# Kernel tuning notes

Measured on AMD Instinct MI355X. Metric: run time of the kernel, lower is better.

## Reference

```python
import jax, jax.numpy as jnp
import numpy as np

D_MODEL = 2048
D_STATE = 64
D_CONV = 4
EXPAND = 2
HEADDIM = 64
NGROUPS = 1
CHUNK = 64
D_INNER = EXPAND * D_MODEL            # 4096
NHEADS = D_INNER // HEADDIM           # 64
D_XBC = D_INNER + 2 * NGROUPS * D_STATE
D_IN_PROJ = 2 * D_INNER + 2 * NGROUPS * D_STATE + NHEADS


def setup_inputs():
    key = jax.random.key(0)
    ks = jax.random.split(key, 8)
    B, L = 2, 4096
    u = jax.random.normal(ks[0], (B, L, D_MODEL), jnp.float32)
    W_in = jax.random.normal(ks[1], (D_IN_PROJ, D_MODEL), jnp.float32) * 0.02
    conv_w = jax.random.normal(ks[2], (D_XBC, D_CONV), jnp.float32) * 0.2
    conv_b = jnp.zeros((D_XBC,), jnp.float32)
    dt = jnp.exp(jax.random.uniform(ks[3], (NHEADS,)) * (np.log(0.1) - np.log(0.001)) + np.log(0.001))
    dt = jnp.clip(dt, 1e-4)
    dt_bias = dt + jnp.log(-jnp.expm1(-dt))
    A_log = jnp.log(jax.random.uniform(ks[4], (NHEADS,), minval=1.0, maxval=16.0))
    D_param = jnp.ones((NHEADS,), jnp.float32)
    norm_w = jnp.ones((D_INNER,), jnp.float32)
    W_out = jax.random.normal(ks[5], (D_MODEL, D_INNER), jnp.float32) * 0.02
    return dict(u=u, W_in=W_in, conv_w=conv_w, conv_b=conv_b, dt_bias=dt_bias,
                A_log=A_log, D_param=D_param, norm_w=norm_w, W_out=W_out)


def segsum(x):
    # x: (..., T) -> (..., T, T) with entry [l,s] = sum_{s< i <= l} x[i], -inf above diag
    T = x.shape[-1]
    mask_strict = jnp.tril(jnp.ones((T, T), bool), k=-1)
    mask_incl = jnp.tril(jnp.ones((T, T), bool), k=0)
    xe = jnp.where(mask_strict, x[..., :, None], 0.0)  # element [l,s] = x[l] if l>s
    xseg = jnp.cumsum(xe, axis=-2)
    return jnp.where(mask_incl, xseg, -jnp.inf)


def ssd_scan(X, A, Bm, Cm, block_len=CHUNK):
    # X: (b,L,h,p), A: (b,L,h), Bm/Cm: (b,L,h,n)
    b, seqlen, h, p = X.shape
    n = Bm.shape[-1]
    pad_len = (block_len - seqlen % block_len) % block_len
    if pad_len > 0:
        X = jnp.pad(X, ((0, 0), (0, pad_len), (0, 0), (0, 0)))
        A = jnp.pad(A, ((0, 0), (0, pad_len), (0, 0)))
        Bm = jnp.pad(Bm, ((0, 0), (0, pad_len), (0, 0), (0, 0)))
        Cm = jnp.pad(Cm, ((0, 0), (0, pad_len), (0, 0), (0, 0)))
    L = X.shape[1]
    c = L // block_len
    Xc = X.reshape(b, c, block_len, h, p)
    Ac = A.reshape(b, c, block_len, h).transpose(0, 3, 1, 2)  # (b,h,c,l)
    Bc = Bm.reshape(b, c, block_len, h, n)
    Cc = Cm.reshape(b, c, block_len, h, n)
    A_cum = jnp.cumsum(Ac, axis=-1)                           # (b,h,c,l)
    Lmat = jnp.exp(segsum(Ac))                                # (b,h,c,l,s)
    CB = jnp.einsum('bclhn,bcshn->bhcls', Cc, Bc)
    Y_diag = jnp.einsum('bhcls,bcshp->bhclp', CB * Lmat, Xc)
    decay_states = jnp.exp(A_cum[..., -1:] - A_cum)           # (b,h,c,l)
    states = jnp.einsum('bhcl,bclhn,bclhp->bhcpn', decay_states, Bc, Xc)
    init = jnp.zeros((b, h, 1, p, n), X.dtype)
    states = jnp.concatenate([init, states], axis=2)          # (b,h,c+1,p,n)
    chunk_decay = jnp.pad(A_cum[..., -1], ((0, 0), (0, 0), (1, 0)))  # (b,h,c+1)
    decay_chunk = jnp.exp(segsum(chunk_decay))                # (b,h,c+1,c+1)
    new_states = jnp.einsum('bhzc,bhcpn->bhzpn', decay_chunk, states)[:, :, :-1]
    Y_off = jnp.einsum('bclhn,bhcpn,bhcl->bhclp', Cc, new_states, jnp.exp(A_cum))
    Y = (Y_diag + Y_off).transpose(0, 2, 3, 1, 4).reshape(b, L, h, p)
    if pad_len > 0:
        Y = Y[:, :seqlen]
    return Y


def rmsnorm_grouped(x, w, ngroups, eps=1e-5):
    gs = x.shape[-1] // ngroups
    xg = x.reshape(*x.shape[:-1], ngroups, gs)
    xg = xg * jax.lax.rsqrt(jnp.mean(xg * xg, axis=-1, keepdims=True) + eps)
    return xg.reshape(x.shape) * w


def reference(u, W_in, conv_w, conv_b, dt_bias, A_log, D_param, norm_w, W_out):
    B, L, _ = u.shape
    zxbcdt = u @ W_in.T                                      # (B,L,d_in_proj)
    z = zxbcdt[..., :D_INNER]
    xBC = zxbcdt[..., D_INNER:D_INNER + D_XBC]
    dt = zxbcdt[..., D_INNER + D_XBC:]
    # causal depthwise conv1d, kernel D_CONV, left-pad D_CONV-1
    xpad = jnp.pad(xBC, ((0, 0), (D_CONV - 1, 0), (0, 0)))
    conv = conv_b
    for k in range(D_CONV):
        conv = conv + conv_w[:, k] * xpad[:, k:k + L, :]
    xBC = jax.nn.silu(conv)
    x = xBC[..., :D_INNER].reshape(B, L, NHEADS, HEADDIM)
    B_ssm = xBC[..., D_INNER:D_INNER + NGROUPS * D_STATE].reshape(B, L, NGROUPS, D_STATE)
    C_ssm = xBC[..., D_INNER + NGROUPS * D_STATE:].reshape(B, L, NGROUPS, D_STATE)
    if NGROUPS < NHEADS:
        rep = NHEADS // NGROUPS
        B_ssm = jnp.repeat(B_ssm, rep, axis=2)
        C_ssm = jnp.repeat(C_ssm, rep, axis=2)
    dt = jax.nn.softplus(dt + dt_bias)                        # (B,L,nheads)
    A = -jnp.exp(A_log)                                       # (nheads,)
    y = ssd_scan(x * dt[..., None], A * dt, B_ssm, C_ssm, block_len=CHUNK)
    y = y + D_param[:, None] * x
    y = y.reshape(B, L, D_INNER)
    y = rmsnorm_grouped(y * jax.nn.silu(z), norm_w, NGROUPS)
    return y @ W_out.T
```

## Files before the change

### kernel.cpp

```cpp
#include <hip/hip_runtime.h>
#include <hip/hip_bf16.h>
#include <math.h>

#define SEQ       4096
#define DMODEL    2048
#define DINNER    4096
#define DXBC      4224
#define NPROJ     8384
#define NHEADS    64
#define HDIM      64
#define DSTATE    64
#define NCHUNK    64
#define XLD       4352

typedef __attribute__((ext_vector_type(8))) _Float16 half8;
typedef __attribute__((ext_vector_type(2))) _Float16 half2v;
typedef __attribute__((ext_vector_type(4))) float floatx4;

__device__ __forceinline__ void async_copy16(void* lds, const void* g) {
  __builtin_amdgcn_global_load_lds(
      (const __attribute__((address_space(1))) unsigned int*)g,
      (__attribute__((address_space(3))) unsigned int*)lds, 16, 0, 0);
}

__device__ __forceinline__ float silu_f(float x) { return x / (1.f + __expf(-x)); }

__device__ __forceinline__ void cvt8(const float* __restrict__ s, _Float16* __restrict__ d) {
  float4 a = *(const float4*)s;
  float4 b = *(const float4*)(s + 4);
  half8 h;
  h[0] = (_Float16)a.x; h[1] = (_Float16)a.y; h[2] = (_Float16)a.z; h[3] = (_Float16)a.w;
  h[4] = (_Float16)b.x; h[5] = (_Float16)b.y; h[6] = (_Float16)b.z; h[7] = (_Float16)b.w;
  *(half8*)d = h;
}

__global__ void diag_kernel(float* out, float v) { out[0] = v; }

__global__ void cvt8_kernel(const float* __restrict__ src, _Float16* __restrict__ dst, int n8) {
  int i = blockIdx.x * 256 + threadIdx.x;
  if (i < n8) cvt8(src + (size_t)i * 8, dst + (size_t)i * 8);
}

#define U_N8 (SEQ * DMODEL / 8)
__global__ void cvt_in_kernel(const float* __restrict__ u, const float* __restrict__ W_in,
                              _Float16* __restrict__ ubf, _Float16* __restrict__ winbf) {
  int i = blockIdx.x * 256 + threadIdx.x;
  if (i < U_N8) {
    cvt8(u + (size_t)i * 8, ubf + (size_t)i * 8);
  } else {
    int j = i - U_N8;
    int row = j >> 8;
    size_t off = (size_t)j * 8;
    if (row < NPROJ) {
      cvt8(W_in + off, winbf + off);
    } else {
      half8 zz = {};
      *(half8*)(winbf + off) = zz;
    }
  }
}

template <typename OT>
__global__ __launch_bounds__(256) void gemm_bt64(
    const _Float16* __restrict__ A, const _Float16* __restrict__ B,
    OT* __restrict__ C0, OT* __restrict__ C1, int K,
    int ldc0, int ldc1, int ncol0, int tiles_m, int tiles_n) {
  __shared__ __align__(16) _Float16 As[128 * 64];
  __shared__ __align__(16) _Float16 Bs[128 * 64];
  int t = threadIdx.x;
  int nt = tiles_m * tiles_n;
  int id = blockIdx.x;
  int id2 = ((nt & 7) == 0) ? ((id & 7) * (nt >> 3) + (id >> 3)) : id;
  int wband = tiles_m << 2;
  int g = id2 / wband;
  int rm = id2 - g * wband;
  int bw = tiles_n - (g << 2); if (bw > 4) bw = 4;
  int pn = (g << 2) + rm % bw;
  int pm = rm / bw;
  int m0 = pm * 128, n0 = pn * 128;

  int w = t >> 6, lane = t & 63, q = lane >> 4, r = lane & 15;
  int wm = (w >> 1) * 64, wn = (w & 1) * 64;
  int rowoff = lane >> 3;
  int chunkoff = ((lane & 7) ^ rowoff) * 8;
  const _Float16* gA[4];
  const _Float16* gB[4];
#pragma unroll
  for (int i = 0; i < 4; ++i) {
    gA[i] = A + (size_t)(m0 + i * 32 + w * 8 + rowoff) * K + chunkoff;
    gB[i] = B + (size_t)(n0 + i * 32 + w * 8 + rowoff) * K + chunkoff;
  }
  floatx4 acc[4][4] = {};
  for (int k0 = 0; k0 < K; k0 += 64) {
#pragma unroll
    for (int i = 0; i < 4; ++i) {
      async_copy16(As + (i * 32 + w * 8) * 64, gA[i] + k0);
      async_copy16(Bs + (i * 32 + w * 8) * 64, gB[i] + k0);
    }
    __syncthreads();
#pragma unroll
    for (int kk = 0; kk < 64; kk += 32) {
      half8 af[4], bf[4];
#pragma unroll
      for (int im = 0; im < 4; ++im) {
        int R = wm + im * 16 + r;
        af[im] = *(const half8*)&As[R * 64 + ((((kk >> 3) + q) ^ (R & 7)) << 3)];
      }
#pragma unroll
      for (int in = 0; in < 4; ++in) {
        int R = wn + in * 16 + r;
        bf[in] = *(const half8*)&Bs[R * 64 + ((((kk >> 3) + q) ^ (R & 7)) << 3)];
      }
#pragma unroll
      for (int im = 0; im < 4; ++im)
#pragma unroll
        for (int in = 0; in < 4; ++in)
          acc[im][in] =
              __builtin_amdgcn_mfma_f32_16x16x32_f16(af[im], bf[in], acc[im][in], 0, 0, 0);
    }
    __syncthreads();
  }
  OT* Cp = (n0 < ncol0) ? C0 : C1;
  int ldc = (n0 < ncol0) ? ldc0 : ldc1;
  int cb = (n0 < ncol0) ? n0 : n0 - ncol0;
#pragma unroll
  for (int im = 0; im < 4; ++im)
#pragma unroll
    for (int in = 0; in < 4; ++in)
#pragma unroll
      for (int i = 0; i < 4; ++i)
        Cp[(size_t)(m0 + wm + im * 16 + q * 4 + i) * ldc + cb + wn + in * 16 + r] =
            (OT)acc[im][in][i];
}

template <typename OT>
__global__ __launch_bounds__(512, 2) void gemm256(
    const _Float16* __restrict__ A, const _Float16* __restrict__ B,
    OT* __restrict__ C, int K, int ldc, int tiles_m, int tiles_n) {
  __shared__ __align__(16) _Float16 As[2][256 * 64];
  __shared__ __align__(16) _Float16 Bs[2][256 * 64];
  int t = threadIdx.x;
  int nwg = tiles_m * tiles_n;
  int id = blockIdx.x;
  int wgid = ((nwg & 7) == 0) ? ((id & 7) * (nwg >> 3) + (id >> 3)) : id;
  int wband = tiles_m << 2;
  int g = wgid / wband;
  int rm = wgid - g * wband;
  int bw = tiles_n - (g << 2); if (bw > 4) bw = 4;
  int pn = (g << 2) + rm % bw;
  int pm = rm / bw;
  int m0 = pm * 256, n0 = pn * 256;

  int w = t >> 6, lane = t & 63, q4 = lane >> 4, r16 = lane & 15;
  int wm = (w >> 2) * 128, wn = (w & 3) * 64;
  int srow = lane >> 3;
  int schunk = ((lane & 7) ^ srow) << 3;
  const _Float16* gA0 = A + (size_t)(m0 + w * 8 + srow) * K + schunk;
  const _Float16* gB0 = B + (size_t)(n0 + w * 8 + srow) * K + schunk;

  floatx4 acc[8][4] = {};

  auto STAGE = [&](int buf, int kt) {
    int k0 = kt << 6;
#pragma unroll
    for (int i = 0; i < 4; ++i) {
      async_copy16(&As[buf][(i * 64 + w * 8) * 64], gA0 + (size_t)(i * 64) * K + k0);
      async_copy16(&Bs[buf][(i * 64 + w * 8) * 64], gB0 + (size_t)(i * 64) * K + k0);
    }
  };

  int NT = K >> 6;
  STAGE(0, 0);
  STAGE(1, 1);
  asm volatile("s_waitcnt vmcnt(8)" ::: "memory");
  __builtin_amdgcn_s_barrier();
  asm volatile("" ::: "memory");

  for (int kt = 0; kt < NT; ++kt) {
    int cur = kt & 1;
    const _Float16* Ab = As[cur];
    const _Float16* Bb = Bs[cur];
#define RD(buf_, R_, kk_) \
  (*(const half8*)&buf_[(R_) * 64 + (((((kk_) >> 3) + q4) ^ ((R_) & 7)) << 3)])
#define PHASE(qm, qn)                                                          \
    {                                                                          \
      half8 af[4][2], bf[2][2];                                                \
      _Pragma("unroll") for (int m = 0; m < 4; ++m) {                          \
        int R = wm + ((qm) * 4 + m) * 16 + r16;                                \
        af[m][0] = RD(Ab, R, 0);                                               \
        af[m][1] = RD(Ab, R, 32);                                              \
      }                                                                        \
      _Pragma("unroll") for (int n = 0; n < 2; ++n) {                          \
        int R = wn + ((qn) * 2 + n) * 16 + r16;                                \
        bf[n][0] = RD(Bb, R, 0);                                               \
        bf[n][1] = RD(Bb, R, 32);                                              \
      }                                                                        \
      __builtin_amdgcn_s_setprio(1);                                           \
      _Pragma("unroll") for (int m = 0; m < 4; ++m)                            \
        _Pragma("unroll") for (int n = 0; n < 2; ++n) {                        \
          acc[(qm) * 4 + m][(qn) * 2 + n] = __builtin_amdgcn_mfma_f32_16x16x32_f16( \
              af[m][0], bf[n][0], acc[(qm) * 4 + m][(qn) * 2 + n], 0, 0, 0);   \
          acc[(qm) * 4 + m][(qn) * 2 + n] = __builtin_amdgcn_mfma_f32_16x16x32_f16( \
              af[m][1], bf[n][1], acc[(qm) * 4 + m][(qn) * 2 + n], 0, 0, 0);   \
        }                                                                      \
      __builtin_amdgcn_s_setprio(0);                                           \
    }
    PHASE(0, 0) PHASE(1, 0) PHASE(1, 1) PHASE(0, 1)
#undef PHASE
#undef RD
    if (kt + 1 < NT) {
      asm volatile("s_waitcnt lgkmcnt(0)" ::: "memory");
      __builtin_amdgcn_s_barrier();
      asm volatile("" ::: "memory");
      if (kt + 2 < NT) {
        STAGE(cur, kt + 2);
        asm volatile("s_waitcnt vmcnt(8)" ::: "memory");
      } else {
        asm volatile("s_waitcnt vmcnt(0)" ::: "memory");
      }
      __builtin_amdgcn_s_barrier();
      asm volatile("" ::: "memory");
    }
  }
#pragma unroll
  for (int m = 0; m < 8; ++m)
#pragma unroll
    for (int n = 0; n < 4; ++n)
#pragma unroll
      for (int i = 0; i < 4; ++i)
        C[(size_t)(m0 + wm + m * 16 + q4 * 4 + i) * ldc + n0 + wn + n * 16 + r16] =
            (OT)acc[m][n][i];
}

#define CONVB (SEQ * (DXBC / 2) / 256)
__global__ __launch_bounds__(256) void conv_dtscan_kernel(
    const _Float16* __restrict__ xin, const float* __restrict__ conv_w,
    const float* __restrict__ conv_b, _Float16* __restrict__ xcv,
    const float* __restrict__ dt_bias, const float* __restrict__ A_log,
    float* __restrict__ dtp, float* __restrict__ acum, float* __restrict__ chs) {
  int t = threadIdx.x;
  if (blockIdx.x < CONVB) {
    int idx = blockIdx.x * 256 + t;
    int l = idx / (DXBC / 2);
    int c = (idx - l * (DXBC / 2)) * 2;
    const _Float16* zc = xin + (size_t)l * XLD + c;
    float a0 = conv_b[c], a1 = conv_b[c + 1];
#pragma unroll
    for (int k = 0; k < 4; ++k) {
      int off = k - 3;
      if (l + off >= 0) {
        half2v v = *(const half2v*)(zc + (long)off * XLD);
        a0 += conv_w[c * 4 + k] * (float)v[0];
        a1 += conv_w[c * 4 + 4 + k] * (float)v[1];
      }
    }
    half2v o;
    o[0] = (_Float16)silu_f(a0);
    o[1] = (_Float16)silu_f(a1);
    *(half2v*)(xcv + (size_t)l * DXBC + c) = o;
  } else {
    __shared__ float dAs[64 * 65];
    int c = blockIdx.x - CONVB;
    int h = t & 63;
    const _Float16* dtraw = xin + DXBC;
    float bias = dt_bias[h];
    float negA = -__expf(A_log[h]);
#pragma unroll
    for (int i = 0; i < 16; ++i) {
      int l = i * 4 + (t >> 6);
      int row = c * 64 + l;
      float x = (float)dtraw[(size_t)row * XLD + h] + bias;
      float dtv = (x > 20.f) ? x : log1pf(__expf(x));
      dtp[(size_t)row * 64 + h] = dtv;
      dAs[l * 65 + h] = negA * dtv;
    }
    __syncthreads();
    if (t < 64) {
      float a = 0.f;
      size_t base = ((size_t)c * 64 + t) * 64;
      for (int l = 0; l < 64; ++l) {
        a += dAs[l * 65 + t];
        acum[base + l] = a;
      }
      chs[c * 64 + t] = a;
    }
  }
}

__global__ __launch_bounds__(256) void states_kernel(
    const _Float16* __restrict__ xcv, const float* __restrict__ dtp,
    const float* __restrict__ acum, const float* __restrict__ chs,
    _Float16* __restrict__ states) {
  int bid = blockIdx.x;
  int c = bid & 63, h = bid >> 6;
  int row0 = c * 64;
  int acbase = (c * 64 + h) * 64;
  __shared__ __align__(16) _Float16 XdT[64 * 72];
  __shared__ __align__(16) _Float16 BdT[64 * 72];
  __shared__ float dec[64];
  int t = threadIdx.x;
  if (t < 64) dec[t] = __expf(chs[acbase >> 6] - acum[acbase + t]);
  __syncthreads();
#pragma unroll
  for (int i = 0; i < 16; ++i) {
    int flat = i * 256 + t;
    int l = flat >> 6, col = flat & 63;
    int grow = row0 + l;
    float dtv = dtp[(size_t)grow * 64 + h];
    float xv = (float)xcv[(size_t)grow * DXBC + h * 64 + col] * dtv;
    XdT[col * 72 + l] = (_Float16)xv;
    float bv = (float)xcv[(size_t)grow * DXBC + DINNER + col] * dec[l];
    BdT[col * 72 + l] = (_Float16)bv;
  }
  __syncthreads();
  int w = t >> 6, lane = t & 63, q = lane >> 4, r = lane & 15;
#pragma unroll
  for (int in = 0; in < 4; ++in) {
    floatx4 a4 = {0.f, 0.f, 0.f, 0.f};
#pragma unroll
    for (int k0 = 0; k0 < 64; k0 += 32) {
      half8 af = *(const half8*)&XdT[(w * 16 + r) * 72 + k0 + q * 8];
      half8 bf = *(const half8*)&BdT[(in * 16 + r) * 72 + k0 + q * 8];
      a4 = __builtin_amdgcn_mfma_f32_16x16x32_f16(af, bf, a4, 0, 0, 0);
    }
#pragma unroll
    for (int i = 0; i < 4; ++i)
      states[((size_t)bid * 64 + (w * 16 + q * 4 + i)) * 64 + in * 16 + r] = (_Float16)a4[i];
  }
}

__global__ __launch_bounds__(256) void scan_kernel(_Float16* __restrict__ states,
                                                   const float* __restrict__ chs) {
  int bid = blockIdx.x;
  int h = bid >> 4, seg = bid & 15;
  size_t base = ((size_t)h * 64) * 4096 + seg * 256 + threadIdx.x;
  float carry = 0.f;
  float s_cur = (float)states[base];
  for (int c = 0; c < 64; ++c) {
    size_t idx = base + (size_t)c * 4096;
    float s_next = (c < 63) ? (float)states[idx + 4096] : 0.f;
    float ec = __expf(chs[c * 64 + h]);
    states[idx] = (_Float16)carry;
    carry = carry * ec + s_cur;
    s_cur = s_next;
  }
}

__global__ __launch_bounds__(256) void yout_kernel(
    const _Float16* __restrict__ xcv, const float* __restrict__ dtp,
    const float* __restrict__ acum, const _Float16* __restrict__ sin_,
    const float* __restrict__ Dp, _Float16* __restrict__ Y) {
  int bid = blockIdx.x;
  int c = bid & 63, h = bid >> 6;
  int row0 = c * 64;
  int acbase = (c * 64 + h) * 64;
  __shared__ __align__(16) _Float16 Cs[64 * 72];
  __shared__ __align__(16) _Float16 Bt[64 * 72];
  __shared__ __align__(16) _Float16 XdT[64 * 72];
  __shared__ __align__(16) _Float16 Ms[64 * 72];
  __shared__ float acs[64];
  int t = threadIdx.x;
  if (t < 64) acs[t] = acum[acbase + t];
#pragma unroll
  for (int i = 0; i < 16; ++i) {
    int flat = i * 256 + t;
    int l = flat >> 6, col = flat & 63;
    int grow = row0 + l;
    const _Float16* rp = xcv + (size_t)grow * DXBC;
    Cs[l * 72 + col] = rp[DINNER + DSTATE + col];
    Bt[l * 72 + col] = rp[DINNER + col];
    float xv = (float)rp[h * 64 + col] * dtp[(size_t)grow * 64 + h];
    XdT[col * 72 + l] = (_Float16)xv;
  }
  __syncthreads();
  int w = t >> 6, lane = t & 63, q = lane >> 4, r = lane & 15;
  int m = w * 16 + r;
#pragma unroll
  for (int in = 0; in < 4; ++in) {
    floatx4 cb = {0.f, 0.f, 0.f, 0.f};
#pragma unroll
    for (int k0 = 0; k0 < 64; k0 += 32) {
      half8 af = *(const half8*)&Cs[m * 72 + k0 + q * 8];
      half8 bf = *(const half8*)&Bt[(in * 16 + r) * 72 + k0 + q * 8];
      cb = __builtin_amdgcn_mfma_f32_16x16x32_f16(af, bf, cb, 0, 0, 0);
    }
#pragma unroll
    for (int i = 0; i < 4; ++i) {
      int l = w * 16 + q * 4 + i;
      int s = in * 16 + r;
      float v = (s <= l) ? cb[i] * __expf(acs[l] - acs[s]) : 0.f;
      Ms[l * 72 + s] = (_Float16)v;
    }
  }
  __syncthreads();
  size_t sbase = (size_t)bid * 4096;
  float Dh = Dp[h];
#pragma unroll
  for (int in = 0; in < 4; ++in) {
    floatx4 acc = {0.f, 0.f, 0.f, 0.f};
#pragma unroll
    for (int k0 = 0; k0 < 64; k0 += 32) {
      half8 af = *(const half8*)&Cs[m * 72 + k0 + q * 8];
      half8 bf = *(const half8*)&sin_[sbase + (size_t)(in * 16 + r) * 64 + k0 + q * 8];
      acc = __builtin_amdgcn_mfma_f32_16x16x32_f16(af, bf, acc, 0, 0, 0);
    }
#pragma unroll
    for (int i = 0; i < 4; ++i) acc[i] *= __expf(acs[w * 16 + q * 4 + i]);
#pragma unroll
    for (int k0 = 0; k0 < 64; k0 += 32) {
      half8 af = *(const half8*)&Ms[m * 72 + k0 + q * 8];
      half8 bf = *(const half8*)&XdT[(in * 16 + r) * 72 + k0 + q * 8];
      acc = __builtin_amdgcn_mfma_f32_16x16x32_f16(af, bf, acc, 0, 0, 0);
    }
#pragma unroll
    for (int i = 0; i < 4; ++i) {
      int l = w * 16 + q * 4 + i;
      int p = in * 16 + r;
      int grow = row0 + l;
      float xv = (float)xcv[(size_t)grow * DXBC + h * 64 + p];
      Y[(size_t)grow * DINNER + h * 64 + p] = (_Float16)(acc[i] + Dh * xv);
    }
  }
}

__global__ __launch_bounds__(256) void rmsnorm_kernel(const _Float16* __restrict__ Y,
                                                      _Float16* __restrict__ Z,
                                                      const float* __restrict__ norm_w) {
  int row = blockIdx.x;
  const half8* y8 = (const half8*)(Y + (size_t)row * DINNER);
  half8* z8 = (half8*)(Z + (size_t)row * DINNER);
  __shared__ float red[4];
  int t = threadIdx.x;
  float g[16];
  float ss = 0.f;
#pragma unroll
  for (int i = 0; i < 2; ++i) {
    int j = i * 256 + t;
    half8 yv = y8[j];
    half8 zv = z8[j];
#pragma unroll
    for (int e = 0; e < 8; ++e) {
      float gv = (float)yv[e] * silu_f((float)zv[e]);
      g[i * 8 + e] = gv;
      ss += gv * gv;
    }
  }
#pragma unroll
  for (int o = 32; o > 0; o >>= 1) ss += __shfl_down(ss, o, 64);
  if ((t & 63) == 0) red[t >> 6] = ss;
  __syncthreads();
  float rs = rsqrtf((red[0] + red[1] + red[2] + red[3]) / (float)DINNER + 1e-5f);
#pragma unroll
  for (int i = 0; i < 2; ++i) {
    int j = i * 256 + t;
    const float4* w4 = (const float4*)(norm_w + j * 8);
    float4 wa = w4[0], wb = w4[1];
    half8 o;
    o[0] = (_Float16)(g[i * 8 + 0] * rs * wa.x);
    o[1] = (_Float16)(g[i * 8 + 1] * rs * wa.y);
    o[2] = (_Float16)(g[i * 8 + 2] * rs * wa.z);
    o[3] = (_Float16)(g[i * 8 + 3] * rs * wa.w);
    o[4] = (_Float16)(g[i * 8 + 4] * rs * wb.x);
    o[5] = (_Float16)(g[i * 8 + 5] * rs * wb.y);
    o[6] = (_Float16)(g[i * 8 + 6] * rs * wb.z);
    o[7] = (_Float16)(g[i * 8 + 7] * rs * wb.w);
    z8[j] = o;
  }
}

extern "C" void kernel_launch(void* const* d_in, const int* in_sizes, int n_in,
                              void* d_out, int out_size, void* d_ws, size_t ws_size,
                              hipStream_t stream) {
  const float* u       = (const float*)d_in[0];
  const float* W_in    = (const float*)d_in[1];
  const float* conv_w  = (const float*)d_in[2];
  const float* conv_b  = (const float*)d_in[3];
  const float* dt_bias = (const float*)d_in[4];
  const float* A_log   = (const float*)d_in[5];
  const float* D_param = (const float*)d_in[6];
  const float* norm_w  = (const float*)d_in[7];
  const float* W_out   = (const float*)d_in[8];
  float* out = (float*)d_out;
  char* ws = (char*)d_ws;

  const size_t NEED_MID   = 192954368ULL;
  const size_t NEED_SMALL = 140525568ULL;
  bool big = (ws_size >= NEED_MID);
  if (!big && ws_size < NEED_SMALL) {
    diag_kernel<<<1, 1, 0, stream>>>(out, (float)ws_size);
    return;
  }

  if (big) {
    _Float16* zb     = (_Float16*)(ws + 0);
    _Float16* xbcdtb = (_Float16*)(ws + 67108864ULL);
    _Float16* xcv    = (_Float16*)(ws + 102760448ULL);
    _Float16* winbf  = xcv;
    _Float16* states = (_Float16*)(ws + 137363456ULL);
    _Float16* ubf    = states;
    _Float16* woutbf = (_Float16*)(ws + 170917888ULL);
    float* dtp  = (float*)(ws + 187695104ULL);
    float* acum = (float*)(ws + 188743680ULL);
    float* chs  = (float*)(ws + 189792256ULL);

    cvt8_kernel<<<DMODEL * DINNER / 8 / 256, 256, 0, stream>>>(
        W_out, woutbf, DMODEL * DINNER / 8);

    for (int b = 0; b < 2; ++b) {
      const float* ub = u + (size_t)b * SEQ * DMODEL;
      _Float16* zbb = zb + (size_t)b * SEQ * DINNER;

      cvt_in_kernel<<<U_N8 / 256 + 8448, 256, 0, stream>>>(ub, W_in, ubf, winbf);

      gemm256<_Float16><<<256, 512, 0, stream>>>(ubf, winbf, zbb, DMODEL, DINNER, 16, 16);
      gemm_bt64<_Float16><<<32 * 34, 256, 0, stream>>>(
          ubf, winbf + (size_t)DINNER * DMODEL, xbcdtb, xbcdtb,
          DMODEL, XLD, XLD, 1 << 30, 32, 34);

      conv_dtscan_kernel<<<CONVB + NCHUNK, 256, 0, stream>>>(
          xbcdtb, conv_w, conv_b, xcv, dt_bias, A_log, dtp, acum, chs);

      states_kernel<<<NHEADS * NCHUNK, 256, 0, stream>>>(xcv, dtp, acum, chs, states);
      scan_kernel<<<NHEADS * 16, 256, 0, stream>>>(states, chs);
      yout_kernel<<<NHEADS * NCHUNK, 256, 0, stream>>>(xcv, dtp, acum, states, D_param,
                                                       xbcdtb );

      rmsnorm_kernel<<<SEQ, 256, 0, stream>>>(xbcdtb, zbb, norm_w);
    }

    gemm256<float><<<256, 512, 0, stream>>>(zb, woutbf, out, DINNER, DMODEL, 32, 8);
  } else {
    _Float16* zb     = (_Float16*)(ws + 0);
    _Float16* xbcdtb = (_Float16*)(ws + 33554432ULL);
    _Float16* Yb     = xbcdtb;
    _Float16* xcv    = (_Float16*)(ws + 69206016ULL);
    _Float16* winbf  = xcv;
    _Float16* states = (_Float16*)(ws + 103809024ULL);
    _Float16* ubf    = states;
    _Float16* woutbf = states;
    float* dtp  = (float*)(ws + 137363456ULL);
    float* acum = (float*)(ws + 139460608ULL);
    float* chs  = (float*)(ws + 140509184ULL);

    for (int b = 0; b < 2; ++b) {
      const float* ub = u + (size_t)b * SEQ * DMODEL;
      float* outb = out + (size_t)b * SEQ * DMODEL;

      cvt_in_kernel<<<U_N8 / 256 + 8448, 256, 0, stream>>>(ub, W_in, ubf, winbf);
      gemm_bt64<_Float16><<<32 * 66, 256, 0, stream>>>(
          ubf, winbf, zb, xbcdtb, DMODEL, DINNER, XLD, DINNER, 32, 66);
      conv_dtscan_kernel<<<CONVB + NCHUNK, 256, 0, stream>>>(
          xbcdtb, conv_w, conv_b, xcv, dt_bias, A_log, dtp, acum, chs);
      states_kernel<<<NHEADS * NCHUNK, 256, 0, stream>>>(xcv, dtp, acum, chs, states);
      scan_kernel<<<NHEADS * 16, 256, 0, stream>>>(states, chs);
      yout_kernel<<<NHEADS * NCHUNK, 256, 0, stream>>>(xcv, dtp, acum, states, D_param, Yb);
      rmsnorm_kernel<<<SEQ, 256, 0, stream>>>(Yb, zb, norm_w);
      cvt8_kernel<<<DMODEL * DINNER / 8 / 256, 256, 0, stream>>>(
          W_out, woutbf, DMODEL * DINNER / 8);
      gemm_bt64<float><<<32 * 16, 256, 0, stream>>>(
          zb, woutbf, outb, outb, DINNER, DMODEL, DMODEL, 1 << 30, 32, 16);
    }
  }
}
```

Measured before the change: 1.122 ms.

## Split GEMM tile into half-tiles and interleave staged loads with MFMA quadrants

Restructures the 256x256 GEMM kernel so the A and B tiles are stored as two 128-row halves each. The K-step is split into four quadrant MFMA phases, and each phase overlaps its LDS fragment reads and the async global loads for the next K-tile with compute, separated by barriers. Warps now own interleaved 64x32 sub-blocks in each quadrant instead of one contiguous 128x64 region. The aim is to hide global-load latency better than the old whole-tile double buffer. In exchange it adds many more barriers per iteration and changes the output store pattern.

```diff
diff --git a/kernel.cpp b/kernel.cpp
--- a/kernel.cpp
+++ b/kernel.cpp
@@ -137,8 +137,8 @@
 __global__ __launch_bounds__(512, 2) void gemm256(
     const _Float16* __restrict__ A, const _Float16* __restrict__ B,
     OT* __restrict__ C, int K, int ldc, int tiles_m, int tiles_n) {
-  __shared__ __align__(16) _Float16 As[2][256 * 64];
-  __shared__ __align__(16) _Float16 Bs[2][256 * 64];
+  __shared__ __align__(16) _Float16 As[2][2][128 * 64];
+  __shared__ __align__(16) _Float16 Bs[2][2][128 * 64];
   int t = threadIdx.x;
   int nwg = tiles_m * tiles_n;
   int id = blockIdx.x;
@@ -152,84 +152,124 @@
   int m0 = pm * 256, n0 = pn * 256;
 
   int w = t >> 6, lane = t & 63, q4 = lane >> 4, r16 = lane & 15;
-  int wm = (w >> 2) * 128, wn = (w & 3) * 64;
   int srow = lane >> 3;
   int schunk = ((lane & 7) ^ srow) << 3;
-  const _Float16* gA0 = A + (size_t)(m0 + w * 8 + srow) * K + schunk;
-  const _Float16* gB0 = B + (size_t)(n0 + w * 8 + srow) * K + schunk;
-
-  floatx4 acc[8][4] = {};
-
-  auto STAGE = [&](int buf, int kt) {
-    int k0 = kt << 6;
-#pragma unroll
-    for (int i = 0; i < 4; ++i) {
-      async_copy16(&As[buf][(i * 64 + w * 8) * 64], gA0 + (size_t)(i * 64) * K + k0);
-      async_copy16(&Bs[buf][(i * 64 + w * 8) * 64], gB0 + (size_t)(i * 64) * K + k0);
-    }
-  };
+  const _Float16* gAb = A + (size_t)(m0 + w * 8 + srow) * K + schunk;
+  const _Float16* gBb = B + (size_t)(n0 + w * 8 + srow) * K + schunk;
+  int Ra = (w >> 2) * 64 + r16;
+  int Rb = (w & 3) * 32 + r16;
+
+  floatx4 acc[4][4][2] = {};
+  half8 af[4][2], bf[2][2];
+
+#define STAGE_A(buf_, H_, kt_)                                                 \
+  {                                                                            \
+    _Pragma("unroll") for (int i_ = 0; i_ < 2; ++i_)                           \
+        async_copy16(&As[buf_][H_][(i_ * 64 + w * 8) * 64],                    \
+                     gAb + (size_t)((H_)*128 + i_ * 64) * K + ((kt_) << 6));   \
+  }
+#define STAGE_B(buf_, H_, kt_)                                                 \
+  {                                                                            \
+    _Pragma("unroll") for (int i_ = 0; i_ < 2; ++i_)                           \
+        async_copy16(&Bs[buf_][H_][(i_ * 64 + w * 8) * 64],                    \
+                     gBb + (size_t)((H_)*128 + i_ * 64) * K + ((kt_) << 6));   \
+  }
+#define LDA(half_)                                                             \
+  _Pragma("unroll") for (int m_ = 0; m_ < 4; ++m_)                             \
+  _Pragma("unroll") for (int k_ = 0; k_ < 2; ++k_) {                           \
+    int R_ = Ra + m_ * 16;                                                     \
+    af[m_][k_] = *(const half8*)&As[cur][half_]                                \
+        [R_ * 64 + (((k_ * 4 + q4) ^ (R_ & 7)) << 3)];                         \
+  }
+#define LDB(half_)                                                             \
+  _Pragma("unroll") for (int n_ = 0; n_ < 2; ++n_)                             \
+  _Pragma("unroll") for (int k_ = 0; k_ < 2; ++k_) {                           \
+    int R_ = Rb + n_ * 16;                                                     \
+    bf[n_][k_] = *(const half8*)&Bs[cur][half_]                                \
+        [R_ * 64 + (((k_ * 4 + q4) ^ (R_ & 7)) << 3)];                         \
+  }
+#define MM(sq_)                                                                \
+  __builtin_amdgcn_s_setprio(1);                                               \
+  _Pragma("unroll") for (int m_ = 0; m_ < 4; ++m_)                             \
+  _Pragma("unroll") for (int n_ = 0; n_ < 2; ++n_)                             \
+  _Pragma("unroll") for (int k_ = 0; k_ < 2; ++k_)                             \
+      acc[sq_][m_][n_] = __builtin_amdgcn_mfma_f32_16x16x32_f16(               \
+          af[m_][k_], bf[n_][k_], acc[sq_][m_][n_], 0, 0, 0);                  \
+  __builtin_amdgcn_s_setprio(0);
+#define BARF() { __builtin_amdgcn_s_barrier(); asm volatile("" ::: "memory"); }
+#define WAITLGKM()                                                             \
+  {                                                                            \
+    asm volatile("s_waitcnt lgkmcnt(0)" ::: "memory");                         \
+    __builtin_amdgcn_sched_barrier(0);                                         \
+  }
 
   int NT = K >> 6;
-  STAGE(0, 0);
-  STAGE(1, 1);
-  asm volatile("s_waitcnt vmcnt(8)" ::: "memory");
-  __builtin_amdgcn_s_barrier();
-  asm volatile("" ::: "memory");
+  STAGE_A(0, 0, 0);
+  STAGE_B(0, 0, 0);
+  STAGE_B(0, 1, 0);
+  STAGE_A(0, 1, 0);
+  asm volatile("s_waitcnt vmcnt(2)" ::: "memory");
+  BARF();
 
   for (int kt = 0; kt < NT; ++kt) {
-    int cur = kt & 1;
-    const _Float16* Ab = As[cur];
-    const _Float16* Bb = Bs[cur];
-#define RD(buf_, R_, kk_) \
-  (*(const half8*)&buf_[(R_) * 64 + (((((kk_) >> 3) + q4) ^ ((R_) & 7)) << 3)])
-#define PHASE(qm, qn)                                                          \
-    {                                                                          \
-      half8 af[4][2], bf[2][2];                                                \
-      _Pragma("unroll") for (int m = 0; m < 4; ++m) {                          \
-        int R = wm + ((qm) * 4 + m) * 16 + r16;                                \
-        af[m][0] = RD(Ab, R, 0);                                               \
-        af[m][1] = RD(Ab, R, 32);                                              \
-      }                                                                        \
-      _Pragma("unroll") for (int n = 0; n < 2; ++n) {                          \
-        int R = wn + ((qn) * 2 + n) * 16 + r16;                                \
-        bf[n][0] = RD(Bb, R, 0);                                               \
-        bf[n][1] = RD(Bb, R, 32);                                              \
-      }                                                                        \
-      __builtin_amdgcn_s_setprio(1);                                           \
-      _Pragma("unroll") for (int m = 0; m < 4; ++m)                            \
-        _Pragma("unroll") for (int n = 0; n < 2; ++n) {                        \
-          acc[(qm) * 4 + m][(qn) * 2 + n] = __builtin_amdgcn_mfma_f32_16x16x32_f16( \
-              af[m][0], bf[n][0], acc[(qm) * 4 + m][(qn) * 2 + n], 0, 0, 0);   \
-          acc[(qm) * 4 + m][(qn) * 2 + n] = __builtin_amdgcn_mfma_f32_16x16x32_f16( \
-              af[m][1], bf[n][1], acc[(qm) * 4 + m][(qn) * 2 + n], 0, 0, 0);   \
-        }                                                                      \
-      __builtin_amdgcn_s_setprio(0);                                           \
-    }
-    PHASE(0, 0) PHASE(1, 0) PHASE(1, 1) PHASE(0, 1)
-#undef PHASE
-#undef RD
-    if (kt + 1 < NT) {
-      asm volatile("s_waitcnt lgkmcnt(0)" ::: "memory");
-      __builtin_amdgcn_s_barrier();
-      asm volatile("" ::: "memory");
-      if (kt + 2 < NT) {
-        STAGE(cur, kt + 2);
-        asm volatile("s_waitcnt vmcnt(8)" ::: "memory");
-      } else {
-        asm volatile("s_waitcnt vmcnt(0)" ::: "memory");
-      }
-      __builtin_amdgcn_s_barrier();
-      asm volatile("" ::: "memory");
-    }
-  }
-#pragma unroll
-  for (int m = 0; m < 8; ++m)
-#pragma unroll
-    for (int n = 0; n < 4; ++n)
-#pragma unroll
-      for (int i = 0; i < 4; ++i)
-        C[(size_t)(m0 + wm + m * 16 + q4 * 4 + i) * ldc + n0 + wn + n * 16 + r16] =
-            (OT)acc[m][n][i];
+    int cur = kt & 1, nxt = cur ^ 1;
+    bool more = (kt + 1 < NT);
+    LDA(0);
+    LDB(0);
+    if (more) STAGE_A(nxt, 0, kt + 1);
+    BARF();
+    WAITLGKM();
+    MM(0);
+    BARF();
+    LDB(1);
+    if (more) {
+      STAGE_B(nxt, 0, kt + 1);
+      asm volatile("s_waitcnt vmcnt(4)" ::: "memory");
+    } else {
+      asm volatile("s_waitcnt vmcnt(0)" ::: "memory");
+    }
+    BARF();
+    WAITLGKM();
+    MM(1);
+    BARF();
+    LDA(1);
+    if (more) STAGE_B(nxt, 1, kt + 1);
+    BARF();
+    WAITLGKM();
+    MM(2);
+    BARF();
+    LDB(0);
+    if (more) {
+      STAGE_A(nxt, 1, kt + 1);
+      asm volatile("s_waitcnt vmcnt(2)" ::: "memory");
+    }
+    BARF();
+    WAITLGKM();
+    MM(3);
+    BARF();
+  }
+
+  const int paC[4] = {0, 0, 1, 1};
+  const int pbC[4] = {0, 1, 1, 0};
+#pragma unroll
+  for (int sq = 0; sq < 4; ++sq) {
+    int rb = m0 + paC[sq] * 128 + (w >> 2) * 64 + q4 * 4;
+    int cb = n0 + pbC[sq] * 128 + (w & 3) * 32 + r16;
+#pragma unroll
+    for (int m = 0; m < 4; ++m)
+#pragma unroll
+      for (int n = 0; n < 2; ++n)
+#pragma unroll
+        for (int i = 0; i < 4; ++i)
+          C[(size_t)(rb + m * 16 + i) * ldc + cb + n * 16] = (OT)acc[sq][m][n][i];
+  }
+#undef STAGE_A
+#undef STAGE_B
+#undef LDA
+#undef LDB
+#undef MM
+#undef BARF
+#undef WAITLGKM
 }
 
 #define CONVB (SEQ * (DXBC / 2) / 256)
```

Measured after the change: 1.092 ms. 2.7% less time.

## Software-pipeline LDS fragment reads in gemm256 and route most in_proj columns through it

Applied to the files above, without the earlier changes.

Restructures the 256x256 GEMM main loop so LDS fragment loads for the next k-half are issued ahead of the MFMAs on the current registers, using double-buffered register fragments and explicit lgkmcnt waits. It also adds a split-output epilogue so one gemm256 launch covers both the z columns and the first 4096 xBC columns of the input projection. Only the remaining 192 columns stay on the smaller 64-tile kernel. The cost is higher register pressure and hand-placed waits and scheduling barriers that may limit compiler scheduling.

```diff
diff --git a/kernel.cpp b/kernel.cpp
--- a/kernel.cpp
+++ b/kernel.cpp
@@ -21,6 +21,14 @@
   __builtin_amdgcn_global_load_lds(
       (const __attribute__((address_space(1))) unsigned int*)g,
       (__attribute__((address_space(3))) unsigned int*)lds, 16, 0, 0);
+}
+
+__device__ __forceinline__ half8 ldsread16(const void* p) {
+  unsigned off = (unsigned)(unsigned long long)
+      (const __attribute__((address_space(3))) void*)p;
+  half8 r;
+  asm volatile("ds_read_b128 %0, %1" : "=v"(r) : "v"(off));
+  return r;
 }
 
 __device__ __forceinline__ float silu_f(float x) { return x / (1.f + __expf(-x)); }
@@ -136,7 +144,8 @@
 template <typename OT>
 __global__ __launch_bounds__(512, 2) void gemm256(
     const _Float16* __restrict__ A, const _Float16* __restrict__ B,
-    OT* __restrict__ C, int K, int ldc, int tiles_m, int tiles_n) {
+    OT* __restrict__ C0, OT* __restrict__ C1, int K,
+    int ldc0, int ldc1, int ncol0, int tiles_m, int tiles_n) {
   __shared__ __align__(16) _Float16 As[2][256 * 64];
   __shared__ __align__(16) _Float16 Bs[2][256 * 64];
   int t = threadIdx.x;
@@ -152,84 +161,108 @@
   int m0 = pm * 256, n0 = pn * 256;
 
   int w = t >> 6, lane = t & 63, q4 = lane >> 4, r16 = lane & 15;
-  int wm = (w >> 2) * 128, wn = (w & 3) * 64;
   int srow = lane >> 3;
   int schunk = ((lane & 7) ^ srow) << 3;
-  const _Float16* gA0 = A + (size_t)(m0 + w * 8 + srow) * K + schunk;
-  const _Float16* gB0 = B + (size_t)(n0 + w * 8 + srow) * K + schunk;
+  const _Float16* gAb = A + (size_t)(m0 + w * 8 + srow) * K + schunk;
+  const _Float16* gBb = B + (size_t)(n0 + w * 8 + srow) * K + schunk;
+  int Ra = (w >> 2) * 128 + r16;
+  int Rb = (w & 3) * 64 + r16;
 
   floatx4 acc[8][4] = {};
-
-  auto STAGE = [&](int buf, int kt) {
-    int k0 = kt << 6;
-#pragma unroll
-    for (int i = 0; i < 4; ++i) {
-      async_copy16(&As[buf][(i * 64 + w * 8) * 64], gA0 + (size_t)(i * 64) * K + k0);
-      async_copy16(&Bs[buf][(i * 64 + w * 8) * 64], gB0 + (size_t)(i * 64) * K + k0);
-    }
-  };
+  half8 afA[4], bfA[4];
+  half8 afB[4], bfB[4];
+
+#define STAGE(buf_, kt_)                                                       \
+  {                                                                            \
+    _Pragma("unroll") for (int i_ = 0; i_ < 4; ++i_)                           \
+        async_copy16(&As[buf_][(i_ * 64 + w * 8) * 64],                        \
+                     gAb + (size_t)(i_ * 64) * K + ((kt_) << 6));              \
+    _Pragma("unroll") for (int i_ = 0; i_ < 4; ++i_)                           \
+        async_copy16(&Bs[buf_][(i_ * 64 + w * 8) * 64],                        \
+                     gBb + (size_t)(i_ * 64) * K + ((kt_) << 6));              \
+  }
+#define LOADP(afX, bfX, buf_, mh_, kh_)                                        \
+  {                                                                            \
+    _Pragma("unroll") for (int mi_ = 0; mi_ < 4; ++mi_) {                      \
+      int R_ = Ra + ((mh_)*4 + mi_) * 16;                                      \
+      afX[mi_] = ldsread16(&As[buf_]                                           \
+          [R_ * 64 + ((((kh_)*4 + q4) ^ (R_ & 7)) << 3)]);                     \
+    }                                                                          \
+    _Pragma("unroll") for (int ni_ = 0; ni_ < 4; ++ni_) {                      \
+      int R_ = Rb + ni_ * 16;                                                  \
+      bfX[ni_] = ldsread16(&Bs[buf_]                                           \
+          [R_ * 64 + ((((kh_)*4 + q4) ^ (R_ & 7)) << 3)]);                     \
+    }                                                                          \
+  }
+#define MMP(afX, bfX, mh_)                                                     \
+  __builtin_amdgcn_s_setprio(1);                                               \
+  _Pragma("unroll") for (int mi_ = 0; mi_ < 4; ++mi_)                          \
+  _Pragma("unroll") for (int ni_ = 0; ni_ < 4; ++ni_)                          \
+      acc[(mh_)*4 + mi_][ni_] = __builtin_amdgcn_mfma_f32_16x16x32_f16(        \
+          afX[mi_], bfX[ni_], acc[(mh_)*4 + mi_][ni_], 0, 0, 0);               \
+  __builtin_amdgcn_s_setprio(0);
+#define BARF() { __builtin_amdgcn_s_barrier(); asm volatile("" ::: "memory"); }
+#define WAIT8()                                                                \
+  {                                                                            \
+    asm volatile("s_waitcnt lgkmcnt(8)" ::: "memory");                         \
+    __builtin_amdgcn_sched_barrier(0);                                         \
+  }
+#define WAIT0()                                                                \
+  {                                                                            \
+    asm volatile("s_waitcnt lgkmcnt(0)" ::: "memory");                         \
+    __builtin_amdgcn_sched_barrier(0);                                         \
+  }
 
   int NT = K >> 6;
   STAGE(0, 0);
   STAGE(1, 1);
   asm volatile("s_waitcnt vmcnt(8)" ::: "memory");
-  __builtin_amdgcn_s_barrier();
-  asm volatile("" ::: "memory");
+  BARF();
+  LOADP(afA, bfA, 0, 0, 0);
 
   for (int kt = 0; kt < NT; ++kt) {
-    int cur = kt & 1;
-    const _Float16* Ab = As[cur];
-    const _Float16* Bb = Bs[cur];
-#define RD(buf_, R_, kk_) \
-  (*(const half8*)&buf_[(R_) * 64 + (((((kk_) >> 3) + q4) ^ ((R_) & 7)) << 3)])
-#define PHASE(qm, qn)                                                          \
-    {                                                                          \
-      half8 af[4][2], bf[2][2];                                                \
-      _Pragma("unroll") for (int m = 0; m < 4; ++m) {                          \
-        int R = wm + ((qm) * 4 + m) * 16 + r16;                                \
-        af[m][0] = RD(Ab, R, 0);                                               \
-        af[m][1] = RD(Ab, R, 32);                                              \
-      }                                                                        \
-      _Pragma("unroll") for (int n = 0; n < 2; ++n) {                          \
-        int R = wn + ((qn) * 2 + n) * 16 + r16;                                \
-        bf[n][0] = RD(Bb, R, 0);                                               \
-        bf[n][1] = RD(Bb, R, 32);                                              \
-      }                                                                        \
-      __builtin_amdgcn_s_setprio(1);                                           \
-      _Pragma("unroll") for (int m = 0; m < 4; ++m)                            \
-        _Pragma("unroll") for (int n = 0; n < 2; ++n) {                        \
-          acc[(qm) * 4 + m][(qn) * 2 + n] = __builtin_amdgcn_mfma_f32_16x16x32_f16( \
-              af[m][0], bf[n][0], acc[(qm) * 4 + m][(qn) * 2 + n], 0, 0, 0);   \
-          acc[(qm) * 4 + m][(qn) * 2 + n] = __builtin_amdgcn_mfma_f32_16x16x32_f16( \
-              af[m][1], bf[n][1], acc[(qm) * 4 + m][(qn) * 2 + n], 0, 0, 0);   \
-        }                                                                      \
-      __builtin_amdgcn_s_setprio(0);                                           \
-    }
-    PHASE(0, 0) PHASE(1, 0) PHASE(1, 1) PHASE(0, 1)
-#undef PHASE
-#undef RD
-    if (kt + 1 < NT) {
-      asm volatile("s_waitcnt lgkmcnt(0)" ::: "memory");
-      __builtin_amdgcn_s_barrier();
-      asm volatile("" ::: "memory");
-      if (kt + 2 < NT) {
-        STAGE(cur, kt + 2);
-        asm volatile("s_waitcnt vmcnt(8)" ::: "memory");
-      } else {
-        asm volatile("s_waitcnt vmcnt(0)" ::: "memory");
-      }
-      __builtin_amdgcn_s_barrier();
-      asm volatile("" ::: "memory");
-    }
-  }
-#pragma unroll
-  for (int m = 0; m < 8; ++m)
-#pragma unroll
-    for (int n = 0; n < 4; ++n)
+    int cur = kt & 1, nxt = cur ^ 1;
+    LOADP(afB, bfB, cur, 1, 0);
+    WAIT8();
+    MMP(afA, bfA, 0);
+    LOADP(afA, bfA, cur, 0, 1);
+    WAIT8();
+    MMP(afB, bfB, 1);
+    LOADP(afB, bfB, cur, 1, 1);
+    WAIT8();
+    MMP(afA, bfA, 0);
+    WAIT0();
+    BARF();
+    if (kt + 2 < NT) {
+      STAGE(cur, kt + 2);
+      asm volatile("s_waitcnt vmcnt(8)" ::: "memory");
+    } else {
+      asm volatile("s_waitcnt vmcnt(0)" ::: "memory");
+    }
+    BARF();
+    if (kt + 1 < NT) LOADP(afA, bfA, nxt, 0, 0);
+    __builtin_amdgcn_sched_barrier(0);
+    MMP(afB, bfB, 1);
+  }
+
+#pragma unroll
+  for (int mi = 0; mi < 8; ++mi) {
+    int rb = m0 + (w >> 2) * 128 + mi * 16 + q4 * 4;
+    OT* Cp = (n0 < ncol0) ? C0 : C1;
+    int ldc = (n0 < ncol0) ? ldc0 : ldc1;
+    int cb0 = ((n0 < ncol0) ? n0 : n0 - ncol0) + (w & 3) * 64 + r16;
+#pragma unroll
+    for (int ni = 0; ni < 4; ++ni)
 #pragma unroll
       for (int i = 0; i < 4; ++i)
-        C[(size_t)(m0 + wm + m * 16 + q4 * 4 + i) * ldc + n0 + wn + n * 16 + r16] =
-            (OT)acc[m][n][i];
+        Cp[(size_t)(rb + i) * ldc + cb0 + ni * 16] = (OT)acc[mi][ni][i];
+  }
+#undef STAGE
+#undef LOADP
+#undef MMP
+#undef BARF
+#undef WAIT8
+#undef WAIT0
 }
 
 #define CONVB (SEQ * (DXBC / 2) / 256)
@@ -512,10 +545,11 @@
 
       cvt_in_kernel<<<U_N8 / 256 + 8448, 256, 0, stream>>>(ub, W_in, ubf, winbf);
 
-      gemm256<_Float16><<<256, 512, 0, stream>>>(ubf, winbf, zbb, DMODEL, DINNER, 16, 16);
-      gemm_bt64<_Float16><<<32 * 34, 256, 0, stream>>>(
-          ubf, winbf + (size_t)DINNER * DMODEL, xbcdtb, xbcdtb,
-          DMODEL, XLD, XLD, 1 << 30, 32, 34);
+      gemm256<_Float16><<<512, 512, 0, stream>>>(
+          ubf, winbf, zbb, xbcdtb, DMODEL, DINNER, XLD, DINNER, 16, 32);
+      gemm_bt64<_Float16><<<64, 256, 0, stream>>>(
+          ubf, winbf + (size_t)2 * DINNER * DMODEL, xbcdtb + DINNER, xbcdtb + DINNER,
+          DMODEL, XLD, XLD, 1 << 30, 32, 2);
 
       conv_dtscan_kernel<<<CONVB + NCHUNK, 256, 0, stream>>>(
           xbcdtb, conv_w, conv_b, xcv, dt_bias, A_log, dtp, acum, chs);
@@ -528,7 +562,8 @@
       rmsnorm_kernel<<<SEQ, 256, 0, stream>>>(xbcdtb, zbb, norm_w);
     }
 
-    gemm256<float><<<256, 512, 0, stream>>>(zb, woutbf, out, DINNER, DMODEL, 32, 8);
+    gemm256<float><<<256, 512, 0, stream>>>(
+        zb, woutbf, out, out, DINNER, DMODEL, DMODEL, 1 << 30, 32, 8);
   } else {
     _Float16* zb     = (_Float16*)(ws + 0);
     _Float16* xbcdtb = (_Float16*)(ws + 33554432ULL);
```

Measured after the change: 1.086 ms. 1.03x faster.
